# Performance work log

Measured on AMD Instinct MI355X. Metric: run time of the kernel, lower is better.

Reference implementation:

```python
import jax, jax.numpy as jnp
import numpy as np

B, S, D, H, DFF = 4, 2048, 1024, 16, 4096
DK = D // H
EPS = 1e-9


def setup_inputs() -> dict:
    key = jax.random.key(0)
    ks = jax.random.split(key, 12)
    s = lambda k, shape, scale: jax.random.normal(k, shape, dtype=jnp.float32) * scale
    return {
        "x": s(ks[0], (B, S, D), 1.0),
        "mask": jnp.ones((B, 1, 1, S), dtype=jnp.int32),
        # Linear weights stored torch-style [out, in]
        "wq": s(ks[1], (D, D), D ** -0.5),
        "wk": s(ks[2], (D, D), D ** -0.5),
        "wv": s(ks[3], (D, D), D ** -0.5),
        "wo": s(ks[4], (D, D), D ** -0.5),
        "w1": s(ks[5], (DFF, D), D ** -0.5),
        "b1": jnp.zeros((DFF,), jnp.float32),
        "w2": s(ks[6], (D, DFF), DFF ** -0.5),
        "b2": jnp.zeros((D,), jnp.float32),
        "g1": jnp.ones((D,), jnp.float32),
        "be1": jnp.zeros((D,), jnp.float32),
        "g2": jnp.ones((D,), jnp.float32),
        "be2": jnp.zeros((D,), jnp.float32),
    }


def _layernorm(x, gamma, beta):
    # Matches AddAndNorm: torch.std uses Bessel correction (ddof=1)
    mean = jnp.mean(x, axis=-1, keepdims=True)
    var = jnp.sum((x - mean) ** 2, axis=-1, keepdims=True) / (x.shape[-1] - 1)
    return gamma * (x - mean) / jnp.sqrt(var + EPS) + beta


def _mha(x, mask, wq, wk, wv, wo):
    b, s, d = x.shape
    def proj(w):  # [b,s,d] @ [d,d]^T -> heads [b,h,s,dk]
        return (x @ w.T).reshape(b, s, H, DK).transpose(0, 2, 1, 3)
    q, k, v = proj(wq), proj(wk), proj(wv)
    scores = jnp.einsum("bhqd,bhkd->bhqk", q, k) / jnp.sqrt(jnp.float32(DK))
    scores = jnp.where(mask == 0, jnp.float32(-1e9), scores)
    attn = jax.nn.softmax(scores, axis=-1)
    out = jnp.einsum("bhqk,bhkd->bhqd", attn, v)
    out = out.transpose(0, 2, 1, 3).reshape(b, s, d)
    return out @ wo.T


def reference(x, mask, wq, wk, wv, wo, w1, b1, w2, b2, g1, be1, g2, be2):
    # Residual 1: x + MHA(LN(x))  (dropout = 0)
    h1 = x + _mha(_layernorm(x, g1, be1), mask, wq, wk, wv, wo)
    # Residual 2: h1 + FFN(LN(h1))
    z = _layernorm(h1, g2, be2)
    ffn = jax.nn.relu(z @ w1.T + b1) @ w2.T + b2
    return h1 + ffn
```

## Files before the change

kernel.cpp:

```cpp
#include <hip/hip_runtime.h>
#include <hip/hip_bf16.h>
#include <cstdint>
#include <cstddef>

typedef __attribute__((ext_vector_type(8))) short short8;
typedef __attribute__((ext_vector_type(4))) float floatx4;
typedef __attribute__((ext_vector_type(4))) unsigned short ushort4e;
typedef __attribute__((ext_vector_type(4))) int intx4;

#define B_   4
#define S_   2048
#define D_   1024
#define H_   16
#define DK_  64
#define DFF_ 4096
#define MTOT (B_ * S_)
#define QKVLD 3072

__device__ __forceinline__ float bf2f(unsigned short u) {
    union { unsigned int i; float f; } v; v.i = ((unsigned int)u) << 16; return v.f;
}
__device__ __forceinline__ unsigned short f2bf(float f) {
    union { float f; unsigned int i; } v; v.f = f;
    unsigned int u = v.i;
    u += 0x7fffu + ((u >> 16) & 1u);
    return (unsigned short)(u >> 16);
}
__device__ __forceinline__ unsigned int pkbf(float a, float b) {
    union { float f; unsigned int u; } x, y; x.f = a; y.f = b;
    return ((x.u + 0x8000u) >> 16) | ((y.u + 0x8000u) & 0xffff0000u);
}
__device__ __forceinline__ void async_cp16(const void* g, void* l) {
    __builtin_amdgcn_global_load_lds(
        (const __attribute__((address_space(1))) unsigned int*)g,
        (__attribute__((address_space(3))) unsigned int*)l,
        16, 0, 0);
}

__global__ void dtype_probe(const unsigned short* __restrict__ x, int* flag) {
    __shared__ float red[4];
    const int tid = threadIdx.x;
    float mx = 0.f;
    #pragma unroll
    for (int i = 0; i < 16; i++) {
        float v = fabsf(bf2f(x[tid * 16 + i]));
        if (v != v) v = 1e30f;
        mx = fmaxf(mx, v);
    }
    #pragma unroll
    for (int off = 32; off > 0; off >>= 1) mx = fmaxf(mx, __shfl_down(mx, off));
    if ((tid & 63) == 0) red[tid >> 6] = mx;
    __syncthreads();
    if (tid == 0) {
        float m = fmaxf(fmaxf(red[0], red[1]), fmaxf(red[2], red[3]));
        *flag = (m > 50.f) ? 1 : 0;
    }
}

__device__ __forceinline__ void cvt8(const void* src, unsigned short* dst, int i, int fl) {
    if (fl) {
        const floatx4* s = (const floatx4*)src;
        floatx4 a = s[i * 2], b = s[i * 2 + 1];
        short8 o;
        o[0] = (short)f2bf(a[0]); o[1] = (short)f2bf(a[1]);
        o[2] = (short)f2bf(a[2]); o[3] = (short)f2bf(a[3]);
        o[4] = (short)f2bf(b[0]); o[5] = (short)f2bf(b[1]);
        o[6] = (short)f2bf(b[2]); o[7] = (short)f2bf(b[3]);
        ((short8*)dst)[i] = o;
    } else {
        ((short8*)dst)[i] = ((const short8*)src)[i];
    }
}

__global__ void cvt_kernel(const void* __restrict__ src,
                           unsigned short* __restrict__ dst,
                           int n8, const int* __restrict__ flag) {
    const int i = blockIdx.x * 256 + threadIdx.x;
    if (i >= n8) return;
    cvt8(src, dst, i, *flag);
}

__global__ void cvt4_kernel(const void* s0, const void* s1, const void* s2, const void* s3,
                            unsigned short* __restrict__ dst,
                            const int* __restrict__ flag) {
    const int t = blockIdx.x >> 9;
    const int i = (blockIdx.x & 511) * 256 + threadIdx.x;
    const void* s = (t == 0) ? s0 : (t == 1) ? s1 : (t == 2) ? s2 : s3;
    cvt8(s, dst + (size_t)t * (D_ * D_), i, *flag);
}

__global__ void cvt_small(const void* b1, const void* b2, const void* g1,
                          const void* be1, const void* g2, const void* be2,
                          unsigned short* db1, unsigned short* db2, unsigned short* dg1,
                          unsigned short* dbe1, unsigned short* dg2, unsigned short* dbe2,
                          const int* __restrict__ flag) {
    const int fl = *flag;
    for (int i = threadIdx.x; i < 1152; i += 256) {
        if (i < 512)       cvt8(b1,  db1,  i,        fl);
        else if (i < 640)  cvt8(b2,  db2,  i - 512,  fl);
        else if (i < 768)  cvt8(g1,  dg1,  i - 640,  fl);
        else if (i < 896)  cvt8(be1, dbe1, i - 768,  fl);
        else if (i < 1024) cvt8(g2,  dg2,  i - 896,  fl);
        else               cvt8(be2, dbe2, i - 1024, fl);
    }
}

#define BM 128
#define BN 128
#define BK 64

template<int RELU, int HAS_BIAS, int RES_MODE, int OUT_MODE>
__global__ __launch_bounds__(256)
void gemm_bt(const unsigned short* __restrict__ A, int lda,
             const unsigned short* __restrict__ W, int ldw,
             const unsigned short* __restrict__ bias,
             const void* resid,
             void* out,
             int M, int N, int K,
             const int* __restrict__ flagp)
{
    __shared__ unsigned short As[BM * BK];
    __shared__ unsigned short Bs[BN * BK];

    const int tid  = threadIdx.x;
    const int lane = tid & 63;
    const int wave = tid >> 6;
    const int wm = wave >> 1;
    const int wn = wave & 1;
    const int lr = lane & 15;
    const int lq = lane >> 4;

    const int m0 = blockIdx.y * BM;
    const int n0 = blockIdx.x * BN;

    int fl = 1;
    if (RES_MODE == 3 || OUT_MODE == 2) fl = *flagp;

    floatx4 acc[4][4];
    #pragma unroll
    for (int i = 0; i < 4; i++)
        #pragma unroll
        for (int j = 0; j < 4; j++)
            acc[i][j] = (floatx4){0.f, 0.f, 0.f, 0.f};

    const int lrow = lane >> 3;
    const int swz  = ((lane & 7) ^ lrow) * 8;
    const int rx   = lr & 7;
    const int p0   = ((lq)     ^ rx) * 8;
    const int p1   = ((4 + lq) ^ rx) * 8;

    for (int k0 = 0; k0 < K; k0 += BK) {
        #pragma unroll
        for (int t = 0; t < 4; t++) {
            const int row = wave * 32 + t * 8;
            async_cp16(A + (size_t)(m0 + row + lrow) * lda + k0 + swz, &As[row * BK]);
            async_cp16(W + (size_t)(n0 + row + lrow) * ldw + k0 + swz, &Bs[row * BK]);
        }
        __syncthreads();
        #pragma unroll
        for (int kk = 0; kk < 2; kk++) {
            const int pos = kk ? p1 : p0;
            short8 af[4], bfr[4];
            #pragma unroll
            for (int i = 0; i < 4; i++) {
                af[i]  = *(const short8*)(&As[(wm * 64 + i * 16 + lr) * BK + pos]);
                bfr[i] = *(const short8*)(&Bs[(wn * 64 + i * 16 + lr) * BK + pos]);
            }
            #pragma unroll
            for (int i = 0; i < 4; i++)
                #pragma unroll
                for (int j = 0; j < 4; j++)
                    acc[i][j] = __builtin_amdgcn_mfma_f32_16x16x32_bf16(
                                    af[i], bfr[j], acc[i][j], 0, 0, 0);
        }
        __syncthreads();
    }

    #pragma unroll
    for (int i = 0; i < 4; i++) {
        #pragma unroll
        for (int j = 0; j < 4; j++) {
            const int col = n0 + wn * 64 + j * 16 + lr;
            const float bv = HAS_BIAS ? bf2f(bias[col]) : 0.f;
            #pragma unroll
            for (int r = 0; r < 4; r++) {
                const int row = m0 + wm * 64 + i * 16 + lq * 4 + r;
                const size_t idx = (size_t)row * N + col;
                float vvv = acc[i][j][r] + bv;
                if (RES_MODE == 1) vvv += bf2f(((const unsigned short*)resid)[idx]);
                if (RES_MODE == 2) vvv += ((const float*)resid)[idx];
                if (RES_MODE == 3) vvv += fl ? ((const float*)resid)[idx]
                                             : bf2f(((const unsigned short*)resid)[idx]);
                if (RELU) vvv = fmaxf(vvv, 0.f);
                if (OUT_MODE == 1)      ((float*)out)[idx] = vvv;
                else if (OUT_MODE == 0) ((unsigned short*)out)[idx] = f2bf(vvv);
                else { if (fl) ((float*)out)[idx] = vvv;
                       else    ((unsigned short*)out)[idx] = f2bf(vvv); }
            }
        }
    }
}

template<int IN_MODE>
__global__ __launch_bounds__(256)
void ln_kernel(const void* __restrict__ Xv,
               const unsigned short* __restrict__ g,
               const unsigned short* __restrict__ be,
               unsigned short* __restrict__ out,
               const int* __restrict__ flagp)
{
    const int row = blockIdx.x;
    const int tid = threadIdx.x;
    int fl = 1;
    if (IN_MODE == 2) fl = *flagp;
    float x4[4];
    if (IN_MODE == 1 || fl) {
        const float* X = (const float*)Xv + (size_t)row * D_ + tid * 4;
        floatx4 t = *(const floatx4*)X;
        x4[0] = t[0]; x4[1] = t[1]; x4[2] = t[2]; x4[3] = t[3];
    } else {
        const unsigned short* X = (const unsigned short*)Xv + (size_t)row * D_ + tid * 4;
        ushort4e u = *(const ushort4e*)X;
        #pragma unroll
        for (int i = 0; i < 4; i++) x4[i] = bf2f(u[i]);
    }
    float s1 = x4[0] + x4[1] + x4[2] + x4[3];
    float s2 = x4[0]*x4[0] + x4[1]*x4[1] + x4[2]*x4[2] + x4[3]*x4[3];
    #pragma unroll
    for (int off = 32; off > 0; off >>= 1) {
        s1 += __shfl_down(s1, off);
        s2 += __shfl_down(s2, off);
    }
    __shared__ float r1[4], r2[4];
    const int wv = tid >> 6;
    if ((tid & 63) == 0) { r1[wv] = s1; r2[wv] = s2; }
    __syncthreads();
    s1 = r1[0] + r1[1] + r1[2] + r1[3];
    s2 = r2[0] + r2[1] + r2[2] + r2[3];
    const float mean = s1 * (1.0f / D_);
    const float var  = (s2 - (float)D_ * mean * mean) * (1.0f / (D_ - 1));
    const float rstd = rsqrtf(var + 1e-9f);

    ushort4e o4;
    #pragma unroll
    for (int i = 0; i < 4; i++) {
        const float gv = bf2f(g[tid * 4 + i]);
        const float bv = bf2f(be[tid * 4 + i]);
        o4[i] = f2bf(gv * (x4[i] - mean) * rstd + bv);
    }
    *(ushort4e*)(out + (size_t)row * D_ + tid * 4) = o4;
}

__global__ __launch_bounds__(256)
void vtrans(const unsigned short* __restrict__ V, int ldv,
            unsigned short* __restrict__ Vt)
{
    __shared__ unsigned short t[64 * 72];
    const int tid = threadIdx.x;
    const int kt  = blockIdx.x * 64;
    const int bh  = blockIdx.y;
    const int b   = bh >> 4, h = bh & 15;
    const int r   = tid >> 2;
    const int c4  = (tid & 3) * 16;
    const unsigned short* vp = V + (size_t)(b * S_ + kt + r) * ldv + h * DK_ + c4;
    *(short8*)&t[r * 72 + c4]     = *(const short8*)vp;
    *(short8*)&t[r * 72 + c4 + 8] = *(const short8*)(vp + 8);
    __syncthreads();
    short8 o0, o1;
    #pragma unroll
    for (int e = 0; e < 8; e++) {
        o0[e] = (short)t[(c4 + e) * 72 + r];
        o1[e] = (short)t[(c4 + 8 + e) * 72 + r];
    }
    unsigned short* op = Vt + ((size_t)bh * DK_ + r) * S_ + kt + c4;
    *(short8*)op       = o0;
    *(short8*)(op + 8) = o1;
}

#define ATK   64
#define KS_LD 64
#define PS_LD 72
#define NT_   (S_ / ATK)

__global__ __launch_bounds__(256)
void attn_mfma(const unsigned short* __restrict__ QKV,
               const unsigned short* __restrict__ Vt,
               const int* __restrict__ mask,
               unsigned short* __restrict__ ctx)
{
    __shared__ unsigned short Ks[2][ATK * KS_LD];
    __shared__ unsigned short Vts[2][DK_ * KS_LD];
    __shared__ unsigned short Ps[4][32 * PS_LD];
    __shared__ float maskadd[S_];
    __shared__ float ared[4][32];

    const int tid  = threadIdx.x;
    const int lane = tid & 63;
    const int w    = tid >> 6;
    const int c    = lane & 15;
    const int qd   = lane >> 4;

    const int flat    = blockIdx.y * gridDim.x + blockIdx.x;
    const int logical = (flat & 7) * 128 + (flat >> 3);
    const int bh   = logical >> 4;
    const int b    = bh >> 4;
    const int h    = bh & 15;
    const int q0   = (logical & 15) * 128 + w * 32;

    const int lrow = lane >> 3;
    const int swz  = ((lane & 7) ^ lrow) * 8;
    const int cx   = c & 7;

    {
        const intx4* mp = (const intx4*)(mask + (size_t)b * S_);
        intx4 m0 = mp[tid * 2];
        intx4 m1 = mp[tid * 2 + 1];
        float* dst = &maskadd[tid * 8];
        dst[0] = (m0[0] == 0) ? -1e9f : 0.f;
        dst[1] = (m0[1] == 0) ? -1e9f : 0.f;
        dst[2] = (m0[2] == 0) ? -1e9f : 0.f;
        dst[3] = (m0[3] == 0) ? -1e9f : 0.f;
        dst[4] = (m1[0] == 0) ? -1e9f : 0.f;
        dst[5] = (m1[1] == 0) ? -1e9f : 0.f;
        dst[6] = (m1[2] == 0) ? -1e9f : 0.f;
        dst[7] = (m1[3] == 0) ? -1e9f : 0.f;
    }

    const float QS = 0.18033688f;
    short8 qf[2][2];
    #pragma unroll
    for (int jq = 0; jq < 2; jq++)
        #pragma unroll
        for (int kk = 0; kk < 2; kk++) {
            const unsigned short* qp =
                QKV + (size_t)(b * S_ + q0 + jq * 16 + c) * QKVLD + h * DK_ + kk * 32 + qd * 8;
            short8 t = *(const short8*)qp;
            short8 o;
            #pragma unroll
            for (int e = 0; e < 8; e++)
                o[e] = (short)f2bf(bf2f((unsigned short)t[e]) * QS);
            qf[jq][kk] = o;
        }

    floatx4 acc_o[2][4];
    #pragma unroll
    for (int iq = 0; iq < 2; iq++)
        #pragma unroll
        for (int jd = 0; jd < 4; jd++)
            acc_o[iq][jd] = (floatx4){0.f, 0.f, 0.f, 0.f};
    float lrun[2] = {0.f, 0.f};

    auto STAGE = [&](int buf, int kt) {
        const unsigned short* kbase =
            QKV + 1024 + (size_t)(b * S_ + kt + w * 16) * QKVLD + h * DK_;
        const unsigned short* vbase =
            Vt + ((size_t)bh * DK_ + w * 16) * S_ + kt;
        #pragma unroll
        for (int t = 0; t < 2; t++) {
            async_cp16(kbase + (size_t)(t * 8 + lrow) * QKVLD + swz,
                       &Ks[buf][(w * 16 + t * 8) * KS_LD]);
            async_cp16(vbase + (size_t)(t * 8 + lrow) * S_ + swz,
                       &Vts[buf][(w * 16 + t * 8) * KS_LD]);
        }
    };

    __syncthreads();
    STAGE(0, 0);

    for (int t = 0; t < NT_; t++) {
        const int cur = t & 1;
        const int kt  = t * ATK;
        if (t + 1 < NT_) {
            STAGE(cur ^ 1, kt + ATK);
            asm volatile("s_waitcnt vmcnt(4)" ::: "memory");
        } else {
            asm volatile("s_waitcnt vmcnt(0)" ::: "memory");
        }
        __builtin_amdgcn_s_barrier();

        floatx4 acc_s[4][2];
        #pragma unroll
        for (int i = 0; i < 4; i++)
            #pragma unroll
            for (int jq = 0; jq < 2; jq++)
                acc_s[i][jq] = (floatx4){0.f, 0.f, 0.f, 0.f};
        #pragma unroll
        for (int kk = 0; kk < 2; kk++) {
            const int pos = ((kk * 4 + qd) ^ cx) * 8;
            short8 kf[4];
            #pragma unroll
            for (int i = 0; i < 4; i++)
                kf[i] = *(const short8*)&Ks[cur][(i * 16 + c) * KS_LD + pos];
            __builtin_amdgcn_s_setprio(1);
            #pragma unroll
            for (int i = 0; i < 4; i++)
                #pragma unroll
                for (int jq = 0; jq < 2; jq++)
                    acc_s[i][jq] = __builtin_amdgcn_mfma_f32_16x16x32_bf16(
                                       kf[i], qf[jq][kk], acc_s[i][jq], 0, 0, 0);
            __builtin_amdgcn_s_setprio(0);
        }

        floatx4 madd[4];
        #pragma unroll
        for (int i = 0; i < 4; i++)
            madd[i] = *(const floatx4*)&maskadd[kt + i * 16 + qd * 4];

        #pragma unroll
        for (int jq = 0; jq < 2; jq++) {
            float ps = 0.f;
            #pragma unroll
            for (int i = 0; i < 4; i++) {
                #pragma unroll
                for (int r = 0; r < 4; r++) {
                    float p = __builtin_amdgcn_exp2f(acc_s[i][jq][r] + madd[i][r]);
                    acc_s[i][jq][r] = p;
                    ps += p;
                }
                uint2 pk;
                pk.x = pkbf(acc_s[i][jq][0], acc_s[i][jq][1]);
                pk.y = pkbf(acc_s[i][jq][2], acc_s[i][jq][3]);
                *(uint2*)&Ps[w][(jq * 16 + c) * PS_LD + i * 16 + qd * 4] = pk;
            }
            ps += __shfl_xor(ps, 16);
            ps += __shfl_xor(ps, 32);
            lrun[jq] += ps;
        }

        #pragma unroll
        for (int kk = 0; kk < 2; kk++) {
            const int pos = ((kk * 4 + qd) ^ cx) * 8;
            short8 pf[2], vf[4];
            #pragma unroll
            for (int iq = 0; iq < 2; iq++)
                pf[iq] = *(const short8*)&Ps[w][(iq * 16 + c) * PS_LD + kk * 32 + qd * 8];
            #pragma unroll
            for (int jd = 0; jd < 4; jd++)
                vf[jd] = *(const short8*)&Vts[cur][(jd * 16 + c) * KS_LD + pos];
            __builtin_amdgcn_s_setprio(1);
            #pragma unroll
            for (int iq = 0; iq < 2; iq++)
                #pragma unroll
                for (int jd = 0; jd < 4; jd++)
                    acc_o[iq][jd] = __builtin_amdgcn_mfma_f32_16x16x32_bf16(
                                        pf[iq], vf[jd], acc_o[iq][jd], 0, 0, 0);
            __builtin_amdgcn_s_setprio(0);
        }

        asm volatile("" ::: "memory");
        __builtin_amdgcn_s_barrier();
    }

    if (lane < 16) { ared[w][c] = 1.f / lrun[0]; ared[w][16 + c] = 1.f / lrun[1]; }
    floatx4 lv0 = *(const floatx4*)&ared[w][qd * 4];
    floatx4 lv1 = *(const floatx4*)&ared[w][16 + qd * 4];
    #pragma unroll
    for (int iq = 0; iq < 2; iq++)
        #pragma unroll
        for (int jd = 0; jd < 4; jd++)
            #pragma unroll
            for (int r = 0; r < 4; r++) {
                const int row = q0 + iq * 16 + qd * 4 + r;
                const int col = h * DK_ + jd * 16 + c;
                const float inv = (iq == 0) ? lv0[r] : lv1[r];
                ctx[(size_t)(b * S_ + row) * D_ + col] = f2bf(acc_o[iq][jd][r] * inv);
            }
}

extern "C" void kernel_launch(void* const* d_in, const int* in_sizes, int n_in,
                              void* d_out, int out_size, void* d_ws, size_t ws_size,
                              hipStream_t stream)
{
    const void* x_raw  = d_in[0];
    const int*  mask   = (const int*)d_in[1];
    const void* wq_raw = d_in[2];
    const void* wk_raw = d_in[3];
    const void* wv_raw = d_in[4];
    const void* wo_raw = d_in[5];
    const void* w1_raw = d_in[6];
    const void* b1_raw = d_in[7];
    const void* w2_raw = d_in[8];
    const void* b2_raw = d_in[9];
    const void* g1_raw = d_in[10];
    const void* be1_raw= d_in[11];
    const void* g2_raw = d_in[12];
    const void* be2_raw= d_in[13];

    char* ws = (char*)d_ws;
    const size_t MB = 1024 * 1024;
    int* flag = (int*)ws;
    unsigned short* cb1  = (unsigned short*)(ws + 1 * 1024);
    unsigned short* cb2  = (unsigned short*)(ws + 16 * 1024);
    unsigned short* cg1  = (unsigned short*)(ws + 32 * 1024);
    unsigned short* cbe1 = (unsigned short*)(ws + 40 * 1024);
    unsigned short* cg2  = (unsigned short*)(ws + 48 * 1024);
    unsigned short* cbe2 = (unsigned short*)(ws + 56 * 1024);
    unsigned short* cwqkvo = (unsigned short*)(ws + 1 * MB);
    unsigned short* cwqkv  = cwqkvo;
    unsigned short* cwo    = cwqkvo + 3 * (D_ * D_);
    unsigned short* cw1  = (unsigned short*)(ws + 9 * MB);
    unsigned short* cw2  = (unsigned short*)(ws + 17 * MB);
    unsigned short* xn1  = (unsigned short*)(ws + 25 * MB);
    unsigned short* ctx  = (unsigned short*)(ws + 25 * MB);
    unsigned short* zbuf = (unsigned short*)(ws + 25 * MB);
    unsigned short* qkv  = (unsigned short*)(ws + 41 * MB);
    float*          h1   = (float*)(ws + 57 * MB);
    unsigned short* vt   = (unsigned short*)d_out;
    unsigned short* xn2  = (unsigned short*)d_out;

    dtype_probe<<<1, 256, 0, stream>>>((const unsigned short*)x_raw, flag);
    cvt_small<<<1, 256, 0, stream>>>(b1_raw, b2_raw, g1_raw, be1_raw, g2_raw, be2_raw,
                                     cb1, cb2, cg1, cbe1, cg2, cbe2, flag);
    cvt4_kernel<<<2048, 256, 0, stream>>>(wq_raw, wk_raw, wv_raw, wo_raw, cwqkvo, flag);
    cvt_kernel<<<(DFF_ * D_ / 8 + 255) / 256, 256, 0, stream>>>(w1_raw, cw1, DFF_ * D_ / 8, flag);
    cvt_kernel<<<(D_ * DFF_ / 8 + 255) / 256, 256, 0, stream>>>(w2_raw, cw2, D_ * DFF_ / 8, flag);

    const dim3 blk(256);
    const dim3 gs(D_ / BN, MTOT / BM);
    const dim3 gsq(QKVLD / BN, MTOT / BM);
    const dim3 gs2(2048 / BN, MTOT / BM);

    ln_kernel<2><<<MTOT, blk, 0, stream>>>(x_raw, cg1, cbe1, xn1, flag);
    gemm_bt<0,0,0,0><<<gsq, blk, 0, stream>>>(xn1, D_, cwqkv, D_, nullptr, nullptr, qkv, MTOT, QKVLD, D_, flag);
    vtrans<<<dim3(S_ / 64, B_ * H_), blk, 0, stream>>>(qkv + 2048, QKVLD, vt);
    attn_mfma<<<dim3(S_ / 128, B_ * H_), blk, 0, stream>>>(qkv, vt, mask, ctx);
    gemm_bt<0,0,3,1><<<gs, blk, 0, stream>>>(ctx, D_, cwo, D_, nullptr, x_raw, h1, MTOT, D_, D_, flag);
    ln_kernel<1><<<MTOT, blk, 0, stream>>>(h1, cg2, cbe2, xn2, flag);
    gemm_bt<1,1,0,0><<<gs2, blk, 0, stream>>>(xn2, D_, cw1, D_, cb1, nullptr, zbuf, MTOT, 2048, D_, flag);
    gemm_bt<0,0,2,1><<<gs, blk, 0, stream>>>(zbuf, 2048, cw2, DFF_, nullptr, h1, h1, MTOT, D_, 2048, flag);
    const unsigned short* w1c = cw1 + (size_t)2048 * D_;
    gemm_bt<1,1,0,0><<<gs2, blk, 0, stream>>>(xn2, D_, w1c, D_, cb1 + 2048, nullptr, zbuf, MTOT, 2048, D_, flag);
    gemm_bt<0,1,2,2><<<gs, blk, 0, stream>>>(zbuf, 2048, cw2 + 2048, DFF_, cb2, h1, d_out, MTOT, D_, 2048, flag);
}
```

Baseline: 604.0 us.

## Load K/V fragments straight from global into registers, drop LDS staging

Removes the double-buffered async LDS staging of K and V tiles in the attention kernel. Each wave now loads its K and V^T MFMA fragments directly from global memory into registers every iteration, which eliminates the block-wide barriers and LDS traffic. It also replaces the software bf16 pack with the hardware v_cvt_pk_bf16_f32 instruction. The trade-off is that each of the four waves now fetches the same K/V tile independently, with no prefetch overlap, so it relies on cache hits and may expose global load latency.

```diff
diff --git a/kernel.cpp b/kernel.cpp
--- a/kernel.cpp
+++ b/kernel.cpp
@@ -25,10 +25,6 @@
     unsigned int u = v.i;
     u += 0x7fffu + ((u >> 16) & 1u);
     return (unsigned short)(u >> 16);
-}
-__device__ __forceinline__ unsigned int pkbf(float a, float b) {
-    union { float f; unsigned int u; } x, y; x.f = a; y.f = b;
-    return ((x.u + 0x8000u) >> 16) | ((y.u + 0x8000u) & 0xffff0000u);
 }
 __device__ __forceinline__ void async_cp16(const void* g, void* l) {
     __builtin_amdgcn_global_load_lds(
@@ -278,7 +274,6 @@
 }
 
 #define ATK   64
-#define KS_LD 64
 #define PS_LD 72
 #define NT_   (S_ / ATK)
 
@@ -288,8 +283,6 @@
                const int* __restrict__ mask,
                unsigned short* __restrict__ ctx)
 {
-    __shared__ unsigned short Ks[2][ATK * KS_LD];
-    __shared__ unsigned short Vts[2][DK_ * KS_LD];
     __shared__ unsigned short Ps[4][32 * PS_LD];
     __shared__ float maskadd[S_];
     __shared__ float ared[4][32];
@@ -306,10 +299,6 @@
     const int b    = bh >> 4;
     const int h    = bh & 15;
     const int q0   = (logical & 15) * 128 + w * 32;
-
-    const int lrow = lane >> 3;
-    const int swz  = ((lane & 7) ^ lrow) * 8;
-    const int cx   = c & 7;
 
     {
         const intx4* mp = (const intx4*)(mask + (size_t)b * S_);
@@ -350,33 +339,27 @@
             acc_o[iq][jd] = (floatx4){0.f, 0.f, 0.f, 0.f};
     float lrun[2] = {0.f, 0.f};
 
-    auto STAGE = [&](int buf, int kt) {
-        const unsigned short* kbase =
-            QKV + 1024 + (size_t)(b * S_ + kt + w * 16) * QKVLD + h * DK_;
-        const unsigned short* vbase =
-            Vt + ((size_t)bh * DK_ + w * 16) * S_ + kt;
-        #pragma unroll
-        for (int t = 0; t < 2; t++) {
-            async_cp16(kbase + (size_t)(t * 8 + lrow) * QKVLD + swz,
-                       &Ks[buf][(w * 16 + t * 8) * KS_LD]);
-            async_cp16(vbase + (size_t)(t * 8 + lrow) * S_ + swz,
-                       &Vts[buf][(w * 16 + t * 8) * KS_LD]);
-        }
-    };
+    const unsigned short* Kbase  = QKV + 1024 + (size_t)(b * S_) * QKVLD + h * DK_;
+    const unsigned short* Vtbase = Vt + (size_t)bh * DK_ * S_;
 
     __syncthreads();
-    STAGE(0, 0);
 
     for (int t = 0; t < NT_; t++) {
-        const int cur = t & 1;
-        const int kt  = t * ATK;
-        if (t + 1 < NT_) {
-            STAGE(cur ^ 1, kt + ATK);
-            asm volatile("s_waitcnt vmcnt(4)" ::: "memory");
-        } else {
-            asm volatile("s_waitcnt vmcnt(0)" ::: "memory");
-        }
-        __builtin_amdgcn_s_barrier();
+        const int kt = t * ATK;
+
+        short8 kf[2][4], vf[2][4];
+        #pragma unroll
+        for (int kk = 0; kk < 2; kk++)
+            #pragma unroll
+            for (int i = 0; i < 4; i++)
+                kf[kk][i] = *(const short8*)(Kbase
+                                + (size_t)(kt + i * 16 + c) * QKVLD + kk * 32 + qd * 8);
+        #pragma unroll
+        for (int kk = 0; kk < 2; kk++)
+            #pragma unroll
+            for (int jd = 0; jd < 4; jd++)
+                vf[kk][jd] = *(const short8*)(Vtbase
+                                + (size_t)(jd * 16 + c) * S_ + kt + kk * 32 + qd * 8);
 
         floatx4 acc_s[4][2];
         #pragma unroll
@@ -384,22 +367,16 @@
             #pragma unroll
             for (int jq = 0; jq < 2; jq++)
                 acc_s[i][jq] = (floatx4){0.f, 0.f, 0.f, 0.f};
-        #pragma unroll
-        for (int kk = 0; kk < 2; kk++) {
-            const int pos = ((kk * 4 + qd) ^ cx) * 8;
-            short8 kf[4];
-            #pragma unroll
-            for (int i = 0; i < 4; i++)
-                kf[i] = *(const short8*)&Ks[cur][(i * 16 + c) * KS_LD + pos];
-            __builtin_amdgcn_s_setprio(1);
+        __builtin_amdgcn_s_setprio(1);
+        #pragma unroll
+        for (int kk = 0; kk < 2; kk++)
             #pragma unroll
             for (int i = 0; i < 4; i++)
                 #pragma unroll
                 for (int jq = 0; jq < 2; jq++)
                     acc_s[i][jq] = __builtin_amdgcn_mfma_f32_16x16x32_bf16(
-                                       kf[i], qf[jq][kk], acc_s[i][jq], 0, 0, 0);
-            __builtin_amdgcn_s_setprio(0);
-        }
+                                       kf[kk][i], qf[jq][kk], acc_s[i][jq], 0, 0, 0);
+        __builtin_amdgcn_s_setprio(0);
 
         floatx4 madd[4];
         #pragma unroll
@@ -411,15 +388,16 @@
             float ps = 0.f;
             #pragma unroll
             for (int i = 0; i < 4; i++) {
+                floatx4 p;
                 #pragma unroll
                 for (int r = 0; r < 4; r++) {
-                    float p = __builtin_amdgcn_exp2f(acc_s[i][jq][r] + madd[i][r]);
-                    acc_s[i][jq][r] = p;
-                    ps += p;
+                    p[r] = __builtin_amdgcn_exp2f(acc_s[i][jq][r] + madd[i][r]);
+                    ps += p[r];
                 }
-                uint2 pk;
-                pk.x = pkbf(acc_s[i][jq][0], acc_s[i][jq][1]);
-                pk.y = pkbf(acc_s[i][jq][2], acc_s[i][jq][3]);
+                unsigned int w0, w1;
+                asm("v_cvt_pk_bf16_f32 %0, %1, %2" : "=v"(w0) : "v"(p[0]), "v"(p[1]));
+                asm("v_cvt_pk_bf16_f32 %0, %1, %2" : "=v"(w1) : "v"(p[2]), "v"(p[3]));
+                uint2 pk; pk.x = w0; pk.y = w1;
                 *(uint2*)&Ps[w][(jq * 16 + c) * PS_LD + i * 16 + qd * 4] = pk;
             }
             ps += __shfl_xor(ps, 16);
@@ -429,26 +407,19 @@
 
         #pragma unroll
         for (int kk = 0; kk < 2; kk++) {
-            const int pos = ((kk * 4 + qd) ^ cx) * 8;
-            short8 pf[2], vf[4];
+            short8 pf[2];
             #pragma unroll
             for (int iq = 0; iq < 2; iq++)
                 pf[iq] = *(const short8*)&Ps[w][(iq * 16 + c) * PS_LD + kk * 32 + qd * 8];
-            #pragma unroll
-            for (int jd = 0; jd < 4; jd++)
-                vf[jd] = *(const short8*)&Vts[cur][(jd * 16 + c) * KS_LD + pos];
             __builtin_amdgcn_s_setprio(1);
             #pragma unroll
             for (int iq = 0; iq < 2; iq++)
                 #pragma unroll
                 for (int jd = 0; jd < 4; jd++)
                     acc_o[iq][jd] = __builtin_amdgcn_mfma_f32_16x16x32_bf16(
-                                        pf[iq], vf[jd], acc_o[iq][jd], 0, 0, 0);
+                                        pf[iq], vf[kk][jd], acc_o[iq][jd], 0, 0, 0);
             __builtin_amdgcn_s_setprio(0);
         }
-
-        asm volatile("" ::: "memory");
-        __builtin_amdgcn_s_barrier();
     }
 
     if (lane < 16) { ared[w][c] = 1.f / lrun[0]; ared[w][16 + c] = 1.f / lrun[1]; }
```

Result: slower. 735.8 us (+21.8%).
